# Optimization experiments

Hardware: AMD Instinct MI355X
Metric: run time of the kernel (lower is better)

## Reference

```python
import jax, jax.numpy as jnp
import numpy as np

VOCAB = 50000
SEQ = 2048
BATCH = 64
D = 256


def setup_inputs() -> dict:
    key = jax.random.key(0)
    ks = jax.random.split(key, 9)
    x = jax.random.randint(ks[0], (SEQ, BATCH), 0, VOCAB)  # token ids, 0 = pad
    emb = jax.random.normal(ks[1], (VOCAB, D), jnp.float32) * 0.02
    emb = emb.at[0].set(0.0)  # padding_idx=0
    idf = jax.random.uniform(ks[2], (VOCAB,), jnp.float32, 0.1, 10.0)
    W1 = jax.random.normal(ks[3], (100, D), jnp.float32) * (1.0 / np.sqrt(D))
    b1 = jax.random.normal(ks[4], (100,), jnp.float32) * 0.01
    W2 = jax.random.normal(ks[5], (150, 100), jnp.float32) * 0.1
    b2 = jax.random.normal(ks[6], (150,), jnp.float32) * 0.01
    W3 = jax.random.normal(ks[7], (2, 150), jnp.float32) * 0.1
    b3 = jax.random.normal(ks[8], (2,), jnp.float32) * 0.01
    return {"x": x, "emb": emb, "idf": idf, "W1": W1, "b1": b1,
            "W2": W2, "b2": b2, "W3": W3, "b3": b3}


def reference(x, emb, idf, W1, b1, W2, b2, W3, b3):
    tokens = x.T  # [B, S] (nums = x.permute(1, 0))
    vocab = emb.shape[0]

    # per-row term frequency: histogram (scatter-add) then gather back
    def tf_row(row):  # row: [S] int
        return jnp.zeros((vocab,), jnp.float32).at[row].add(1.0)[row]

    tf = jax.vmap(tf_row)(tokens)                      # [B, S]
    scores = jnp.where(tokens == 0, 0.0, tf * idf[tokens])  # [B, S]

    # bmm of (B, D, S) with (B, S, 1) == tf-idf weighted sum of embeddings
    pooled = jnp.einsum('bsd,bs->bd', emb[tokens], scores)  # [B, D]

    h = jax.nn.relu(pooled @ W1.T + b1)
    h = jax.nn.relu(h @ W2.T + b2)
    return jax.nn.softmax(h @ W3.T + b3, axis=-1)  # [B, 2]
```

## Files before the change

### kernel.cpp

```cpp
#include <hip/hip_runtime.h>

#define VOCAB 50000
#define SEQ   2048
#define BATCH 64
#define DIM   256
#define H1    100
#define H2    150
#define HASH  4096
#define NCH   8
#define CHUNK (SEQ / NCH)
#define NT    1024
#define NWAVE (NT / 64)

__global__ __launch_bounds__(1024)
void k_scores(const int* __restrict__ x,
              const float* __restrict__ idf,
              int2* __restrict__ pairs) {
    __shared__ int tok[SEQ];
    __shared__ int hkey[HASH];
    __shared__ int hcnt[HASH];
    const int r = blockIdx.x;
    const int t = threadIdx.x;

    for (int i = t; i < HASH; i += NT) { hkey[i] = -1; hcnt[i] = 0; }
#pragma unroll
    for (int n = 0; n < SEQ / NT; ++n) {
        const int s = n * NT + t;
        tok[s] = x[s * BATCH + r];
    }
    __syncthreads();

#pragma unroll
    for (int n = 0; n < SEQ / NT; ++n) {
        const int s = n * NT + t;
        const int mytok = tok[s];
        unsigned h = ((unsigned)mytok * 2654435761u) >> 20;
        while (true) {
            int prev = atomicCAS(&hkey[h], -1, mytok);
            if (prev == -1 || prev == mytok) { atomicAdd(&hcnt[h], 1); break; }
            h = (h + 1) & (HASH - 1);
        }
    }
    __syncthreads();

#pragma unroll
    for (int n = 0; n < SEQ / NT; ++n) {
        const int s = n * NT + t;
        const int mytok = tok[s];
        unsigned h = ((unsigned)mytok * 2654435761u) >> 20;
        while (hkey[h] != mytok) h = (h + 1) & (HASH - 1);
        const float sc = (mytok == 0) ? 0.0f : (float)hcnt[h] * idf[mytok];
        pairs[(size_t)r * SEQ + s] = make_int2(mytok, __float_as_int(sc));
    }
}

__global__ __launch_bounds__(1024)
void k_gather(const int2* __restrict__ pairs,
              const float* __restrict__ emb,
              float* __restrict__ partials) {
    __shared__ int   ctok[CHUNK];
    __shared__ float csc[CHUNK];
    __shared__ float wacc[NWAVE][DIM];

    const int bx = blockIdx.x;
    const int r  = bx >> 3;
    const int c  = bx & (NCH - 1);
    const int t  = threadIdx.x;
    const int w  = t >> 6, lane = t & 63;

    if (t < CHUNK) {
        const int2 p = pairs[(size_t)r * SEQ + c * CHUNK + t];
        ctok[t] = p.x;
        csc[t]  = __int_as_float(p.y);
    }
    __syncthreads();

    {
        const float4* embv = (const float4*)emb;
        float4 acc = make_float4(0.f, 0.f, 0.f, 0.f);
        const int i0 = w * (CHUNK / NWAVE);
#pragma unroll
        for (int i = 0; i < CHUNK / NWAVE; ++i) {
            const float sv = csc[i0 + i];
            const float4 v = embv[(size_t)ctok[i0 + i] * (DIM / 4) + lane];
            acc.x = fmaf(v.x, sv, acc.x);
            acc.y = fmaf(v.y, sv, acc.y);
            acc.z = fmaf(v.z, sv, acc.z);
            acc.w = fmaf(v.w, sv, acc.w);
        }
        ((float4*)wacc[w])[lane] = acc;
    }
    __syncthreads();

    if (t < DIM) {
        float a = 0.0f;
#pragma unroll
        for (int i = 0; i < NWAVE; ++i) a += wacc[i][t];
        partials[(size_t)bx * DIM + t] = a;
    }
}

__global__ __launch_bounds__(1024)
void k_mlp(const float* __restrict__ partials,
           const float* __restrict__ W1, const float* __restrict__ b1,
           const float* __restrict__ W2, const float* __restrict__ b2,
           const float* __restrict__ W3, const float* __restrict__ b3,
           float* __restrict__ out) {
    __shared__ float pooled[DIM];
    __shared__ float hp1[128][4];
    __shared__ float h1s[112];
    __shared__ float hp2[H2][4];
    __shared__ float h2s[152];
    __shared__ float lg[2];
    const int r = blockIdx.x;
    const int t = threadIdx.x;

    if (t < DIM) {
        float a = 0.0f;
#pragma unroll
        for (int cc = 0; cc < NCH; ++cc)
            a += partials[((size_t)r * NCH + cc) * DIM + t];
        pooled[t] = a;
    }
    __syncthreads();

    if (t < 512) {
        const int j = t >> 2;
        const int q = t & 3;
        if (j < H1) {
            const float4* wv = (const float4*)(W1 + j * DIM + q * 64);
            const float4* pv = ((const float4*)pooled) + q * 16;
            float a = 0.0f;
#pragma unroll
            for (int i = 0; i < 16; ++i) {
                const float4 ww = wv[i];
                const float4 pp = pv[i];
                a += ww.x * pp.x + ww.y * pp.y + ww.z * pp.z + ww.w * pp.w;
            }
            hp1[j][q] = a;
        }
    }
    __syncthreads();
    if (t < H1)
        h1s[t] = fmaxf(hp1[t][0] + hp1[t][1] + hp1[t][2] + hp1[t][3] + b1[t], 0.0f);
    __syncthreads();

    if (t < 600) {
        const int j = t >> 2;
        const int q = t & 3;
        const float* wv = W2 + j * H1 + q * 25;
        float a = 0.0f;
#pragma unroll
        for (int i = 0; i < 25; ++i)
            a = fmaf(wv[i], h1s[q * 25 + i], a);
        hp2[j][q] = a;
    }
    __syncthreads();
    if (t < H2)
        h2s[t] = fmaxf(hp2[t][0] + hp2[t][1] + hp2[t][2] + hp2[t][3] + b2[t], 0.0f);
    __syncthreads();

    if (t < 2) {
        const float* wv = W3 + t * H2;
        float a = b3[t];
        for (int k = 0; k < H2; ++k) a = fmaf(wv[k], h2s[k], a);
        lg[t] = a;
    }
    __syncthreads();
    if (t == 0) {
        const float m  = fmaxf(lg[0], lg[1]);
        const float e0 = __expf(lg[0] - m);
        const float e1 = __expf(lg[1] - m);
        const float inv = 1.0f / (e0 + e1);
        out[r * 2 + 0] = e0 * inv;
        out[r * 2 + 1] = e1 * inv;
    }
}

extern "C" void kernel_launch(void* const* d_in, const int* in_sizes, int n_in,
                              void* d_out, int out_size, void* d_ws, size_t ws_size,
                              hipStream_t stream) {
    const int*   x   = (const int*)  d_in[0];
    const float* emb = (const float*)d_in[1];
    const float* idf = (const float*)d_in[2];
    const float* W1  = (const float*)d_in[3];
    const float* b1  = (const float*)d_in[4];
    const float* W2  = (const float*)d_in[5];
    const float* b2  = (const float*)d_in[6];
    const float* W3  = (const float*)d_in[7];
    const float* b3  = (const float*)d_in[8];
    float* out = (float*)d_out;

    int2*  pairs    = (int2*)d_ws;
    float* partials = (float*)((char*)d_ws + (size_t)BATCH * SEQ * sizeof(int2));

    k_scores<<<BATCH, NT, 0, stream>>>(x, idf, pairs);
    k_gather<<<BATCH * NCH, NT, 0, stream>>>(pairs, emb, partials);
    k_mlp   <<<BATCH, NT, 0, stream>>>(partials, W1, b1, W2, b2, W3, b3, out);
}
```

Baseline: 127.8 us.

## Fuse score computation into gather kernel with redundant per-chunk histogram

Merges the histogram/score kernel into the gather kernel. Each of the 8 chunk blocks per row rebuilds the full-row hash histogram in shared memory, then computes scores for its own chunk. This removes one kernel launch and the pairs workspace round-trip through global memory. In exchange the histogram work is repeated eight times per row. Shared memory per block also grows, which may reduce occupancy. Emb indexing switches to 32-bit unsigned arithmetic.

```diff
diff --git a/kernel.cpp b/kernel.cpp
--- a/kernel.cpp
+++ b/kernel.cpp
@@ -13,14 +13,22 @@
 #define NWAVE (NT / 64)
 
 __global__ __launch_bounds__(1024)
-void k_scores(const int* __restrict__ x,
+void k_gather(const int* __restrict__ x,
+              const float* __restrict__ emb,
               const float* __restrict__ idf,
-              int2* __restrict__ pairs) {
-    __shared__ int tok[SEQ];
-    __shared__ int hkey[HASH];
-    __shared__ int hcnt[HASH];
-    const int r = blockIdx.x;
-    const int t = threadIdx.x;
+              float* __restrict__ partials) {
+    __shared__ int   tok[SEQ];
+    __shared__ int   hkey[HASH];
+    __shared__ int   hcnt[HASH];
+    __shared__ float sc[CHUNK];
+    __shared__ float wacc[NWAVE][DIM];
+
+    const int bx = blockIdx.x;
+    const int r  = bx >> 3;
+    const int c  = bx & (NCH - 1);
+    const int t  = threadIdx.x;
+    const int w  = t >> 6, lane = t & 63;
+    const int s0 = c * CHUNK;
 
     for (int i = t; i < HASH; i += NT) { hkey[i] = -1; hcnt[i] = 0; }
 #pragma unroll
@@ -43,35 +51,12 @@
     }
     __syncthreads();
 
-#pragma unroll
-    for (int n = 0; n < SEQ / NT; ++n) {
-        const int s = n * NT + t;
+    if (t < CHUNK) {
+        const int s = s0 + t;
         const int mytok = tok[s];
         unsigned h = ((unsigned)mytok * 2654435761u) >> 20;
         while (hkey[h] != mytok) h = (h + 1) & (HASH - 1);
-        const float sc = (mytok == 0) ? 0.0f : (float)hcnt[h] * idf[mytok];
-        pairs[(size_t)r * SEQ + s] = make_int2(mytok, __float_as_int(sc));
-    }
-}
-
-__global__ __launch_bounds__(1024)
-void k_gather(const int2* __restrict__ pairs,
-              const float* __restrict__ emb,
-              float* __restrict__ partials) {
-    __shared__ int   ctok[CHUNK];
-    __shared__ float csc[CHUNK];
-    __shared__ float wacc[NWAVE][DIM];
-
-    const int bx = blockIdx.x;
-    const int r  = bx >> 3;
-    const int c  = bx & (NCH - 1);
-    const int t  = threadIdx.x;
-    const int w  = t >> 6, lane = t & 63;
-
-    if (t < CHUNK) {
-        const int2 p = pairs[(size_t)r * SEQ + c * CHUNK + t];
-        ctok[t] = p.x;
-        csc[t]  = __int_as_float(p.y);
+        sc[t] = (mytok == 0) ? 0.0f : (float)hcnt[h] * idf[mytok];
     }
     __syncthreads();
 
@@ -81,8 +66,9 @@
         const int i0 = w * (CHUNK / NWAVE);
 #pragma unroll
         for (int i = 0; i < CHUNK / NWAVE; ++i) {
-            const float sv = csc[i0 + i];
-            const float4 v = embv[(size_t)ctok[i0 + i] * (DIM / 4) + lane];
+            const float sv = sc[i0 + i];
+            const unsigned idx = (unsigned)tok[s0 + i0 + i] * 64u + (unsigned)lane;
+            const float4 v = embv[idx];
             acc.x = fmaf(v.x, sv, acc.x);
             acc.y = fmaf(v.y, sv, acc.y);
             acc.z = fmaf(v.z, sv, acc.z);
@@ -191,10 +177,8 @@
     const float* b3  = (const float*)d_in[8];
     float* out = (float*)d_out;
 
-    int2*  pairs    = (int2*)d_ws;
-    float* partials = (float*)((char*)d_ws + (size_t)BATCH * SEQ * sizeof(int2));
+    float* partials = (float*)d_ws;
 
-    k_scores<<<BATCH, NT, 0, stream>>>(x, idf, pairs);
-    k_gather<<<BATCH * NCH, NT, 0, stream>>>(pairs, emb, partials);
+    k_gather<<<BATCH * NCH, NT, 0, stream>>>(x, emb, idf, partials);
     k_mlp   <<<BATCH, NT, 0, stream>>>(partials, W1, b1, W2, b2, W3, b3, out);
 }
```

Measured after the change: 127.3 us. No clear change (-0.4%).
